# Kernel tuning notes

Hardware: AMD Instinct MI355X
Metric: run time of the kernel (lower is better)

The kernel has to match this reference:

```python
import jax, jax.numpy as jnp
import numpy as np

LN_EPS = 1e-5
BN_EPS = 1e-5


def setup_inputs() -> dict:
    key = jax.random.key(0)
    ks = jax.random.split(key, 16)
    b, n = 16, 256
    sc = 0.1
    inp = {
        "x": jax.random.normal(ks[0], (b, n, 4), jnp.float32),
        # proj: Linear(4, 64)
        "proj_w": jax.random.normal(ks[1], (4, 64), jnp.float32) * sc,
        "proj_b": jnp.zeros((64,), jnp.float32),
        # sigma_net: Linear(128,64) -> LayerNorm(64) -> ReLU -> Linear(64,1) -> Softplus
        "s_w1": jax.random.normal(ks[2], (128, 64), jnp.float32) * sc,
        "s_b1": jnp.zeros((64,), jnp.float32),
        "ln_g": jnp.ones((64,), jnp.float32),
        "ln_b": jnp.zeros((64,), jnp.float32),
        "s_w2": jax.random.normal(ks[3], (64, 1), jnp.float32) * sc,
        "s_b2": jnp.zeros((1,), jnp.float32),
        # gnn weight
        "gnn_w": jax.random.normal(ks[4], (64, 64), jnp.float32) * sc,
        # classifier: Linear(128,64) -> BatchNorm1d(64) -> ELU -> Dropout(eval) -> Linear(64,2)
        "c_w1": jax.random.normal(ks[5], (128, 64), jnp.float32) * sc,
        "c_b1": jnp.zeros((64,), jnp.float32),
        "bn_g": jnp.ones((64,), jnp.float32),
        "bn_b": jnp.zeros((64,), jnp.float32),
        "bn_mean": jnp.zeros((64,), jnp.float32),
        "bn_var": jnp.ones((64,), jnp.float32),
        "c_w2": jax.random.normal(ks[6], (64, 2), jnp.float32) * sc,
        "c_b2": jnp.zeros((2,), jnp.float32),
    }
    return inp


def reference(x, proj_w, proj_b, s_w1, s_b1, ln_g, ln_b, s_w2, s_b2,
              gnn_w, c_w1, c_b1, bn_g, bn_b, bn_mean, bn_var, c_w2, c_b2):
    # h: [b, n, 64]
    h = jax.nn.elu(x @ proj_w + proj_b)

    # sigma_net(cat([xi, xj])) == hi @ s_w1[:64] + hj @ s_w1[64:] + s_b1, broadcast pairwise
    a_i = h @ s_w1[:64]            # [b, n, 64]
    a_j = h @ s_w1[64:]            # [b, n, 64]
    pre = a_i[:, :, None, :] + a_j[:, None, :, :] + s_b1  # [b, n, n, 64]
    mu = jnp.mean(pre, axis=-1, keepdims=True)
    var = jnp.mean((pre - mu) ** 2, axis=-1, keepdims=True)
    ln = (pre - mu) * jax.lax.rsqrt(var + LN_EPS) * ln_g + ln_b
    sig_pre = jax.nn.relu(ln) @ s_w2 + s_b2               # [b, n, n, 1]
    sigmas = jax.nn.softplus(sig_pre[..., 0])             # [b, n, n]

    # squared pairwise distance via gram trick: ||hi - hj||^2
    sq = jnp.sum(h * h, axis=-1)                          # [b, n]
    gram = jnp.einsum("bid,bjd->bij", h, h)               # [b, n, n]
    d2 = jnp.maximum(sq[:, :, None] + sq[:, None, :] - 2.0 * gram, 0.0)
    adj = jnp.exp(-d2 / (2.0 * sigmas ** 2 + 1e-6))       # [b, n, n]

    h_agg = jnp.einsum("bij,bjd->bid", adj, h) @ gnn_w    # [b, n, 64]
    h_res = jax.nn.elu(h_agg + h)

    pooled = jnp.concatenate([h_res.mean(axis=1), h_res.max(axis=1)], axis=1)  # [b, 128]

    z = pooled @ c_w1 + c_b1
    z = (z - bn_mean) * jax.lax.rsqrt(bn_var + BN_EPS) * bn_g + bn_b  # BN eval mode
    z = jax.nn.elu(z)                                      # Dropout is identity in eval
    return z @ c_w2 + c_b2                                 # [b, 2]
```

## Files before the change

kernel.cpp:

```cpp
#include <hip/hip_runtime.h>
#include <math.h>

#define OFF_H      0
#define OFF_AI     262144
#define OFF_AJH    524288
#define OFF_SAI    1048576
#define OFF_QAI    1052672
#define OFF_SAJ    1056768
#define OFF_QAJ    1060864
#define OFF_SQH    1064960
#define OFF_HRES   1069056

__device__ __forceinline__ float fexp(float x)  { return __expf(x); }
__device__ __forceinline__ float flog(float x)  { return __logf(x); }
__device__ __forceinline__ float frcp(float x)  {
    float r = __builtin_amdgcn_rcpf(x);
    return r * (2.f - x * r);
}
__device__ __forceinline__ float frsq(float x)  { return __builtin_amdgcn_rsqf(x); }

__device__ __forceinline__ float elu_f(float x) { return x > 0.f ? x : fexp(x) - 1.f; }
__device__ __forceinline__ float softplus_f(float x) {
    return fmaxf(x, 0.f) + flog(1.f + fexp(-fabsf(x)));
}

__global__ __launch_bounds__(256) void k1_embed(
    const float* __restrict__ x,
    const float* __restrict__ proj_w, const float* __restrict__ proj_b,
    const float* __restrict__ s_w1, const float* __restrict__ s_b1,
    float* __restrict__ h, float* __restrict__ a_i, float2* __restrict__ ajh,
    float* __restrict__ sa_i, float* __restrict__ qa_i,
    float* __restrict__ sa_j, float* __restrict__ qa_j,
    float* __restrict__ sqh)
{
    __shared__ float w_sh[8192];
    int tid = threadIdx.x;
    #pragma unroll
    for (int r = 0; r < 8; ++r)
        *(float4*)&w_sh[(r*256 + tid)*4] = *(const float4*)&s_w1[(r*256 + tid)*4];
    __syncthreads();

    int lane = tid & 63;
    int wave = tid >> 6;
    int row0 = blockIdx.x * 8;

    float pw0 = proj_w[lane], pw1 = proj_w[64+lane], pw2 = proj_w[128+lane],
          pw3 = proj_w[192+lane], pb = proj_b[lane], b1 = s_b1[lane];

    #pragma unroll
    for (int r = 0; r < 2; ++r) {
        int row = row0 + wave*2 + r;
        int b = row >> 8, i = row & 255;
        float4 xv = *(const float4*)&x[row*4];
        float hv = elu_f(xv.x*pw0 + xv.y*pw1 + xv.z*pw2 + xv.w*pw3 + pb);

        float ai = b1, aj = 0.f;
        #pragma unroll 8
        for (int e = 0; e < 64; ++e) {
            float he = __shfl(hv, e);
            ai = fmaf(he, w_sh[e*64 + lane], ai);
            aj = fmaf(he, w_sh[(64+e)*64 + lane], aj);
        }
        h[row*64 + lane]   = hv;
        a_i[row*64 + lane] = ai;
        ajh[b*16384 + lane*256 + i] = make_float2(aj, hv);

        float v1 = ai, v2 = ai*ai, v3 = aj, v4 = aj*aj, v5 = hv*hv;
        #pragma unroll
        for (int off = 32; off > 0; off >>= 1) {
            v1 += __shfl_xor(v1, off);
            v2 += __shfl_xor(v2, off);
            v3 += __shfl_xor(v3, off);
            v4 += __shfl_xor(v4, off);
            v5 += __shfl_xor(v5, off);
        }
        if (lane == 0) {
            sa_i[row] = v1; qa_i[row] = v2;
            sa_j[row] = v3; qa_j[row] = v4;
            sqh[row]  = v5;
        }
    }
}

__global__ __launch_bounds__(256) void k2_pair(
    const float* __restrict__ a_i, const float2* __restrict__ ajh,
    const float* __restrict__ h,
    const float* __restrict__ sa_i, const float* __restrict__ qa_i,
    const float* __restrict__ sa_j, const float* __restrict__ qa_j,
    const float* __restrict__ sqh,
    const float* __restrict__ ln_g, const float* __restrict__ ln_b,
    const float* __restrict__ s_w2, const float* __restrict__ s_b2,
    const float* __restrict__ gnn_w,
    float* __restrict__ h_res)
{
    int bi0 = blockIdx.x * 4;
    int b   = bi0 >> 8;
    int j   = threadIdx.x;
    int gj  = b*256 + j;

    __shared__ float aiT[64][4], hiT[64][4];
    __shared__ float gbw[64][4];
    __shared__ float sai_s[4], qai_s[4], sqi_s[4];
    __shared__ float adj_sh[256][4];
    __shared__ float pool[16*4*64];
    __shared__ float hagg_sh[4][64];

    {
        int i = j >> 6, d = j & 63;
        aiT[d][i] = a_i[(bi0+i)*64 + d];
        hiT[d][i] = h[(bi0+i)*64 + d];
    }
    if (j < 64) {
        gbw[j][0] = ln_g[j]; gbw[j][1] = ln_b[j]; gbw[j][2] = s_w2[j]; gbw[j][3] = 0.f;
    }
    if (j < 4) {
        sai_s[j] = sa_i[bi0+j]; qai_s[j] = qa_i[bi0+j]; sqi_s[j] = sqh[bi0+j];
    }
    float saj = sa_j[gj], qaj = qa_j[gj], sqj = sqh[gj];
    float b2  = s_b2[0];
    __syncthreads();

    const float2* ajhb = ajh + b*16384;

    float ga[4] = {0.f,0.f,0.f,0.f}, gh[4] = {0.f,0.f,0.f,0.f};
    #pragma unroll 8
    for (int d = 0; d < 64; ++d) {
        float2 v = ajhb[d*256 + j];
        float4 A = *(const float4*)&aiT[d][0];
        float4 H = *(const float4*)&hiT[d][0];
        ga[0] = fmaf(A.x, v.x, ga[0]); ga[1] = fmaf(A.y, v.x, ga[1]);
        ga[2] = fmaf(A.z, v.x, ga[2]); ga[3] = fmaf(A.w, v.x, ga[3]);
        gh[0] = fmaf(H.x, v.y, gh[0]); gh[1] = fmaf(H.y, v.y, gh[1]);
        gh[2] = fmaf(H.z, v.y, gh[2]); gh[3] = fmaf(H.w, v.y, gh[3]);
    }

    float rs4[4], nr4[4], d24[4];
    #pragma unroll
    for (int i = 0; i < 4; ++i) {
        float mu  = (sai_s[i] + saj) * (1.f/64.f);
        float pss = qai_s[i] + qaj + 2.f*ga[i];
        float var = pss * (1.f/64.f) - mu*mu;
        rs4[i] = frsq(var + 1e-5f);
        nr4[i] = -mu * rs4[i];
        d24[i] = fmaxf(sqi_s[i] + sqj - 2.f*gh[i], 0.f);
    }

    float acc[4] = {0.f,0.f,0.f,0.f};
    #pragma unroll 8
    for (int d = 0; d < 64; ++d) {
        float ajd = ajhb[d*256 + j].x;
        float4 A = *(const float4*)&aiT[d][0];
        float4 G = *(const float4*)&gbw[d][0];
        float t0 = fmaxf(fmaf(fmaf(A.x + ajd, rs4[0], nr4[0]), G.x, G.y), 0.f);
        acc[0] = fmaf(t0, G.z, acc[0]);
        float t1 = fmaxf(fmaf(fmaf(A.y + ajd, rs4[1], nr4[1]), G.x, G.y), 0.f);
        acc[1] = fmaf(t1, G.z, acc[1]);
        float t2 = fmaxf(fmaf(fmaf(A.z + ajd, rs4[2], nr4[2]), G.x, G.y), 0.f);
        acc[2] = fmaf(t2, G.z, acc[2]);
        float t3 = fmaxf(fmaf(fmaf(A.w + ajd, rs4[3], nr4[3]), G.x, G.y), 0.f);
        acc[3] = fmaf(t3, G.z, acc[3]);
    }

    {
        float4 av;
        #pragma unroll
        for (int i = 0; i < 4; ++i) {
            float sig = softplus_f(acc[i] + b2);
            float inv = frcp(2.f*sig*sig + 1e-6f);
            ((float*)&av)[i] = fexp(-d24[i] * inv);
        }
        *(float4*)&adj_sh[j][0] = av;
    }
    __syncthreads();

    {
        int q = j >> 4, dq = j & 15;
        const float* hb = h + b*256*64;
        float4 p0 = {0.f,0.f,0.f,0.f}, p1 = p0, p2 = p0, p3 = p0;
        #pragma unroll
        for (int k = 0; k < 16; ++k) {
            int jj = q*16 + k;
            float4 hv = *(const float4*)&hb[jj*64 + dq*4];
            float4 a4 = *(const float4*)&adj_sh[jj][0];
            p0.x=fmaf(a4.x,hv.x,p0.x); p0.y=fmaf(a4.x,hv.y,p0.y);
            p0.z=fmaf(a4.x,hv.z,p0.z); p0.w=fmaf(a4.x,hv.w,p0.w);
            p1.x=fmaf(a4.y,hv.x,p1.x); p1.y=fmaf(a4.y,hv.y,p1.y);
            p1.z=fmaf(a4.y,hv.z,p1.z); p1.w=fmaf(a4.y,hv.w,p1.w);
            p2.x=fmaf(a4.z,hv.x,p2.x); p2.y=fmaf(a4.z,hv.y,p2.y);
            p2.z=fmaf(a4.z,hv.z,p2.z); p2.w=fmaf(a4.z,hv.w,p2.w);
            p3.x=fmaf(a4.w,hv.x,p3.x); p3.y=fmaf(a4.w,hv.y,p3.y);
            p3.z=fmaf(a4.w,hv.z,p3.z); p3.w=fmaf(a4.w,hv.w,p3.w);
        }
        *(float4*)&pool[(q*4 + 0)*64 + dq*4] = p0;
        *(float4*)&pool[(q*4 + 1)*64 + dq*4] = p1;
        *(float4*)&pool[(q*4 + 2)*64 + dq*4] = p2;
        *(float4*)&pool[(q*4 + 3)*64 + dq*4] = p3;
    }
    __syncthreads();

    {
        int i = j >> 6, d = j & 63;
        float s = 0.f;
        #pragma unroll
        for (int q2 = 0; q2 < 16; ++q2)
            s += pool[(q2*4 + i)*64 + d];
        hagg_sh[i][d] = s;
    }
    __syncthreads();

    {
        int i = j >> 6, lane = j & 63;
        float accg = 0.f;
        #pragma unroll 8
        for (int e = 0; e < 64; ++e)
            accg = fmaf(hagg_sh[i][e], gnn_w[e*64 + lane], accg);
        h_res[(bi0+i)*64 + lane] = elu_f(accg + hiT[lane][i]);
    }
}

__global__ __launch_bounds__(256) void k4_pool_cls(
    const float* __restrict__ h_res,
    const float* __restrict__ c_w1, const float* __restrict__ c_b1,
    const float* __restrict__ bn_g, const float* __restrict__ bn_b,
    const float* __restrict__ bn_mean, const float* __restrict__ bn_var,
    const float* __restrict__ c_w2, const float* __restrict__ c_b2,
    float* __restrict__ out)
{
    int b = blockIdx.x;
    int tid = threadIdx.x;
    int d = tid & 63, q = tid >> 6;
    const float* hb = h_res + b*256*64;

    float sum = 0.f, mx = -INFINITY;
    #pragma unroll 8
    for (int k = 0; k < 64; ++k) {
        float v = hb[(q*64+k)*64 + d];
        sum += v; mx = fmaxf(mx, v);
    }
    __shared__ float sum_sh[256], max_sh[256];
    __shared__ float pm_sh[64], px_sh[64];
    sum_sh[tid] = sum; max_sh[tid] = mx;
    __syncthreads();
    if (tid < 64) {
        float tsum = sum_sh[tid] + sum_sh[64+tid] + sum_sh[128+tid] + sum_sh[192+tid];
        float tmax = fmaxf(fmaxf(max_sh[tid], max_sh[64+tid]),
                           fmaxf(max_sh[128+tid], max_sh[192+tid]));
        pm_sh[tid] = tsum * (1.f/256.f);
        px_sh[tid] = tmax;
    }
    __syncthreads();
    if (tid < 64) {
        float acc = c_b1[tid];
        #pragma unroll
        for (int e = 0; e < 64; ++e) {
            acc += pm_sh[e] * c_w1[e*64 + tid];
            acc += px_sh[e] * c_w1[(64+e)*64 + tid];
        }
        float z = (acc - bn_mean[tid]) * rsqrtf(bn_var[tid] + 1e-5f) * bn_g[tid] + bn_b[tid];
        z = elu_f(z);
        float c0 = z * c_w2[tid*2 + 0];
        float c1 = z * c_w2[tid*2 + 1];
        for (int off = 32; off > 0; off >>= 1) {
            c0 += __shfl_down(c0, off);
            c1 += __shfl_down(c1, off);
        }
        if (tid == 0) {
            out[b*2 + 0] = c0 + c_b2[0];
            out[b*2 + 1] = c1 + c_b2[1];
        }
    }
}

extern "C" void kernel_launch(void* const* d_in, const int* in_sizes, int n_in,
                              void* d_out, int out_size, void* d_ws, size_t ws_size,
                              hipStream_t stream) {
    const float* x       = (const float*)d_in[0];
    const float* proj_w  = (const float*)d_in[1];
    const float* proj_b  = (const float*)d_in[2];
    const float* s_w1    = (const float*)d_in[3];
    const float* s_b1    = (const float*)d_in[4];
    const float* ln_g    = (const float*)d_in[5];
    const float* ln_b    = (const float*)d_in[6];
    const float* s_w2    = (const float*)d_in[7];
    const float* s_b2    = (const float*)d_in[8];
    const float* gnn_w   = (const float*)d_in[9];
    const float* c_w1    = (const float*)d_in[10];
    const float* c_b1    = (const float*)d_in[11];
    const float* bn_g    = (const float*)d_in[12];
    const float* bn_b    = (const float*)d_in[13];
    const float* bn_mean = (const float*)d_in[14];
    const float* bn_var  = (const float*)d_in[15];
    const float* c_w2    = (const float*)d_in[16];
    const float* c_b2    = (const float*)d_in[17];

    float* w = (float*)d_ws;
    float*  h     = w + OFF_H;
    float*  a_i   = w + OFF_AI;
    float2* ajh   = (float2*)(w + OFF_AJH);
    float*  sa_i  = w + OFF_SAI;
    float*  qa_i  = w + OFF_QAI;
    float*  sa_j  = w + OFF_SAJ;
    float*  qa_j  = w + OFF_QAJ;
    float*  sqh   = w + OFF_SQH;
    float*  h_res = w + OFF_HRES;
    float*  out   = (float*)d_out;

    k1_embed<<<512, 256, 0, stream>>>(x, proj_w, proj_b, s_w1, s_b1,
                                      h, a_i, ajh,
                                      sa_i, qa_i, sa_j, qa_j, sqh);
    k2_pair<<<1024, 256, 0, stream>>>(a_i, ajh, h,
                                      sa_i, qa_i, sa_j, qa_j, sqh,
                                      ln_g, ln_b, s_w2, s_b2, gnn_w, h_res);
    k4_pool_cls<<<16, 256, 0, stream>>>(h_res, c_w1, c_b1, bn_g, bn_b,
                                        bn_mean, bn_var, c_w2, c_b2, out);
}
```

Baseline: 46.26 us.

## Fuse pooling and classifier into pair kernel via last-blocks atomic handoff

Removes the separate pooling/classifier launch. Each pair block increments a global arrival counter, and the last 16 arriving blocks each take one batch's pooling and classifier. Those blocks spin on a flag that the final arrival sets, so every h_res write is visible before they read it. The counter is reset inside the embed kernel. This saves one kernel launch and its inter-kernel gap, at the cost of a serialized tail where 15 blocks busy-wait for the last block.

```diff
diff --git a/kernel.cpp b/kernel.cpp
--- a/kernel.cpp
+++ b/kernel.cpp
@@ -10,6 +10,7 @@
 #define OFF_QAJ    1060864
 #define OFF_SQH    1064960
 #define OFF_HRES   1069056
+#define OFF_SYNC   1331200
 
 __device__ __forceinline__ float fexp(float x)  { return __expf(x); }
 __device__ __forceinline__ float flog(float x)  { return __logf(x); }
@@ -18,7 +19,6 @@
     return r * (2.f - x * r);
 }
 __device__ __forceinline__ float frsq(float x)  { return __builtin_amdgcn_rsqf(x); }
-
 __device__ __forceinline__ float elu_f(float x) { return x > 0.f ? x : fexp(x) - 1.f; }
 __device__ __forceinline__ float softplus_f(float x) {
     return fmaxf(x, 0.f) + flog(1.f + fexp(-fabsf(x)));
@@ -31,8 +31,10 @@
     float* __restrict__ h, float* __restrict__ a_i, float2* __restrict__ ajh,
     float* __restrict__ sa_i, float* __restrict__ qa_i,
     float* __restrict__ sa_j, float* __restrict__ qa_j,
-    float* __restrict__ sqh)
+    float* __restrict__ sqh, unsigned* __restrict__ sync)
 {
+    if (blockIdx.x == 0 && threadIdx.x == 0) { sync[0] = 0u; sync[1] = 0u; }
+
     __shared__ float w_sh[8192];
     int tid = threadIdx.x;
     #pragma unroll
@@ -91,7 +93,12 @@
     const float* __restrict__ ln_g, const float* __restrict__ ln_b,
     const float* __restrict__ s_w2, const float* __restrict__ s_b2,
     const float* __restrict__ gnn_w,
-    float* __restrict__ h_res)
+    const float* __restrict__ c_w1, const float* __restrict__ c_b1,
+    const float* __restrict__ bn_g, const float* __restrict__ bn_b,
+    const float* __restrict__ bn_mean, const float* __restrict__ bn_var,
+    const float* __restrict__ c_w2, const float* __restrict__ c_b2,
+    float* __restrict__ h_res, unsigned* __restrict__ sync,
+    float* __restrict__ out)
 {
     int bi0 = blockIdx.x * 4;
     int b   = bi0 >> 8;
@@ -104,6 +111,7 @@
     __shared__ float adj_sh[256][4];
     __shared__ float pool[16*4*64];
     __shared__ float hagg_sh[4][64];
+    __shared__ unsigned arrival;
 
     {
         int i = j >> 6, d = j & 63;
@@ -216,57 +224,69 @@
             accg = fmaf(hagg_sh[i][e], gnn_w[e*64 + lane], accg);
         h_res[(bi0+i)*64 + lane] = elu_f(accg + hiT[lane][i]);
     }
-}
-
-__global__ __launch_bounds__(256) void k4_pool_cls(
-    const float* __restrict__ h_res,
-    const float* __restrict__ c_w1, const float* __restrict__ c_b1,
-    const float* __restrict__ bn_g, const float* __restrict__ bn_b,
-    const float* __restrict__ bn_mean, const float* __restrict__ bn_var,
-    const float* __restrict__ c_w2, const float* __restrict__ c_b2,
-    float* __restrict__ out)
-{
-    int b = blockIdx.x;
-    int tid = threadIdx.x;
-    int d = tid & 63, q = tid >> 6;
-    const float* hb = h_res + b*256*64;
-
-    float sum = 0.f, mx = -INFINITY;
-    #pragma unroll 8
-    for (int k = 0; k < 64; ++k) {
-        float v = hb[(q*64+k)*64 + d];
-        sum += v; mx = fmaxf(mx, v);
-    }
-    __shared__ float sum_sh[256], max_sh[256];
-    __shared__ float pm_sh[64], px_sh[64];
-    sum_sh[tid] = sum; max_sh[tid] = mx;
-    __syncthreads();
-    if (tid < 64) {
-        float tsum = sum_sh[tid] + sum_sh[64+tid] + sum_sh[128+tid] + sum_sh[192+tid];
-        float tmax = fmaxf(fmaxf(max_sh[tid], max_sh[64+tid]),
-                           fmaxf(max_sh[128+tid], max_sh[192+tid]));
-        pm_sh[tid] = tsum * (1.f/256.f);
-        px_sh[tid] = tmax;
-    }
-    __syncthreads();
-    if (tid < 64) {
-        float acc = c_b1[tid];
-        #pragma unroll
-        for (int e = 0; e < 64; ++e) {
-            acc += pm_sh[e] * c_w1[e*64 + tid];
-            acc += px_sh[e] * c_w1[(64+e)*64 + tid];
-        }
-        float z = (acc - bn_mean[tid]) * rsqrtf(bn_var[tid] + 1e-5f) * bn_g[tid] + bn_b[tid];
-        z = elu_f(z);
-        float c0 = z * c_w2[tid*2 + 0];
-        float c1 = z * c_w2[tid*2 + 1];
-        for (int off = 32; off > 0; off >>= 1) {
-            c0 += __shfl_down(c0, off);
-            c1 += __shfl_down(c1, off);
-        }
-        if (tid == 0) {
-            out[b*2 + 0] = c0 + c_b2[0];
-            out[b*2 + 1] = c1 + c_b2[1];
+
+    __threadfence();
+    if (j == 0) arrival = atomicAdd(&sync[0], 1u);
+    __syncthreads();
+    unsigned a = arrival;
+    if (a < 1008u) return;
+    int bb = (int)(a - 1008u);
+
+    if (j == 0) {
+        if (a == 1023u) {
+            atomicExch(&sync[1], 1u);
+        } else {
+            while (atomicAdd(&sync[1], 0u) == 0u)
+                __builtin_amdgcn_s_sleep(8);
+        }
+    }
+    __syncthreads();
+    __threadfence();
+
+    {
+        float* sum_sh = pool;
+        float* max_sh = pool + 256;
+        float* pm_sh  = pool + 512;
+        float* px_sh  = pool + 576;
+
+        int d = j & 63, q = j >> 6;
+        const float* hb = h_res + bb*256*64;
+
+        float sum = 0.f, mx = -INFINITY;
+        #pragma unroll 8
+        for (int k = 0; k < 64; ++k) {
+            float v = hb[(q*64+k)*64 + d];
+            sum += v; mx = fmaxf(mx, v);
+        }
+        sum_sh[j] = sum; max_sh[j] = mx;
+        __syncthreads();
+        if (j < 64) {
+            float tsum = sum_sh[j] + sum_sh[64+j] + sum_sh[128+j] + sum_sh[192+j];
+            float tmax = fmaxf(fmaxf(max_sh[j], max_sh[64+j]),
+                               fmaxf(max_sh[128+j], max_sh[192+j]));
+            pm_sh[j] = tsum * (1.f/256.f);
+            px_sh[j] = tmax;
+        }
+        __syncthreads();
+        if (j < 64) {
+            float acc2 = c_b1[j];
+            #pragma unroll
+            for (int e = 0; e < 64; ++e) {
+                acc2 += pm_sh[e] * c_w1[e*64 + j];
+                acc2 += px_sh[e] * c_w1[(64+e)*64 + j];
+            }
+            float z = (acc2 - bn_mean[j]) * rsqrtf(bn_var[j] + 1e-5f) * bn_g[j] + bn_b[j];
+            z = elu_f(z);
+            float c0 = z * c_w2[j*2 + 0];
+            float c1 = z * c_w2[j*2 + 1];
+            for (int off = 32; off > 0; off >>= 1) {
+                c0 += __shfl_down(c0, off);
+                c1 += __shfl_down(c1, off);
+            }
+            if (j == 0) {
+                out[bb*2 + 0] = c0 + c_b2[0];
+                out[bb*2 + 1] = c1 + c_b2[1];
+            }
         }
     }
 }
@@ -294,23 +314,24 @@
     const float* c_b2    = (const float*)d_in[17];
 
     float* w = (float*)d_ws;
-    float*  h     = w + OFF_H;
-    float*  a_i   = w + OFF_AI;
-    float2* ajh   = (float2*)(w + OFF_AJH);
-    float*  sa_i  = w + OFF_SAI;
-    float*  qa_i  = w + OFF_QAI;
-    float*  sa_j  = w + OFF_SAJ;
-    float*  qa_j  = w + OFF_QAJ;
-    float*  sqh   = w + OFF_SQH;
-    float*  h_res = w + OFF_HRES;
-    float*  out   = (float*)d_out;
+    float*    h     = w + OFF_H;
+    float*    a_i   = w + OFF_AI;
+    float2*   ajh   = (float2*)(w + OFF_AJH);
+    float*    sa_i  = w + OFF_SAI;
+    float*    qa_i  = w + OFF_QAI;
+    float*    sa_j  = w + OFF_SAJ;
+    float*    qa_j  = w + OFF_QAJ;
+    float*    sqh   = w + OFF_SQH;
+    float*    h_res = w + OFF_HRES;
+    unsigned* sync  = (unsigned*)(w + OFF_SYNC);
+    float*    out   = (float*)d_out;
 
     k1_embed<<<512, 256, 0, stream>>>(x, proj_w, proj_b, s_w1, s_b1,
                                       h, a_i, ajh,
-                                      sa_i, qa_i, sa_j, qa_j, sqh);
+                                      sa_i, qa_i, sa_j, qa_j, sqh, sync);
     k2_pair<<<1024, 256, 0, stream>>>(a_i, ajh, h,
                                       sa_i, qa_i, sa_j, qa_j, sqh,
-                                      ln_g, ln_b, s_w2, s_b2, gnn_w, h_res);
-    k4_pool_cls<<<16, 256, 0, stream>>>(h_res, c_w1, c_b1, bn_g, bn_b,
-                                        bn_mean, bn_var, c_w2, c_b2, out);
-}
+                                      ln_g, ln_b, s_w2, s_b2, gnn_w,
+                                      c_w1, c_b1, bn_g, bn_b, bn_mean, bn_var,
+                                      c_w2, c_b2, h_res, sync, out);
+}
```

Result: slower. 122.7 us (+165.2%).

## Compute pairwise gram matrices with bf16 MFMA in a separate kernel

Applied to the files above, without the earlier changes.

Adds a kgram kernel that computes the a_i·a_j and h·h gram matrices per batch using bf16 MFMA 16x16x32 instructions, writing two full fp32 [b,n,n] matrices to workspace. k1 now also emits bf16 copies of a_i, a_j and h, and k2 reads the precomputed grams instead of running its own 64-step FMA loop. This trades scalar FMA work for matrix-core work plus an extra launch and roughly 8 MB of extra global traffic. Using bf16 for the variance and distance terms lowers precision and risks cancellation error.

```diff
diff --git a/kernel.cpp b/kernel.cpp
--- a/kernel.cpp
+++ b/kernel.cpp
@@ -9,7 +9,13 @@
 #define OFF_SAJ    1056768
 #define OFF_QAJ    1060864
 #define OFF_SQH    1064960
-#define OFF_HRES   1069056
+#define OFF_GA     1069056
+#define OFF_GH     2117632
+#define OFF_HRES   3166208
+#define OFF_BF     3428352
+
+typedef __attribute__((ext_vector_type(8))) short bf16x8;
+typedef __attribute__((ext_vector_type(4))) float f32x4;
 
 __device__ __forceinline__ float fexp(float x)  { return __expf(x); }
 __device__ __forceinline__ float flog(float x)  { return __logf(x); }
@@ -18,10 +24,14 @@
     return r * (2.f - x * r);
 }
 __device__ __forceinline__ float frsq(float x)  { return __builtin_amdgcn_rsqf(x); }
-
 __device__ __forceinline__ float elu_f(float x) { return x > 0.f ? x : fexp(x) - 1.f; }
 __device__ __forceinline__ float softplus_f(float x) {
     return fmaxf(x, 0.f) + flog(1.f + fexp(-fabsf(x)));
+}
+__device__ __forceinline__ short f2bf(float f) {
+    unsigned u = __float_as_uint(f);
+    unsigned r = (u + 0x7FFF + ((u >> 16) & 1)) >> 16;
+    return (short)r;
 }
 
 __global__ __launch_bounds__(256) void k1_embed(
@@ -29,6 +39,7 @@
     const float* __restrict__ proj_w, const float* __restrict__ proj_b,
     const float* __restrict__ s_w1, const float* __restrict__ s_b1,
     float* __restrict__ h, float* __restrict__ a_i, float2* __restrict__ ajh,
+    short* __restrict__ ai_bf, short* __restrict__ aj_bf, short* __restrict__ h_bf,
     float* __restrict__ sa_i, float* __restrict__ qa_i,
     float* __restrict__ sa_j, float* __restrict__ qa_j,
     float* __restrict__ sqh)
@@ -64,6 +75,9 @@
         h[row*64 + lane]   = hv;
         a_i[row*64 + lane] = ai;
         ajh[b*16384 + lane*256 + i] = make_float2(aj, hv);
+        ai_bf[row*64 + lane] = f2bf(ai);
+        aj_bf[row*64 + lane] = f2bf(aj);
+        h_bf [row*64 + lane] = f2bf(hv);
 
         float v1 = ai, v2 = ai*ai, v3 = aj, v4 = aj*aj, v5 = hv*hv;
         #pragma unroll
@@ -82,9 +96,41 @@
     }
 }
 
+__global__ __launch_bounds__(64) void kgram(
+    const short* __restrict__ ai_bf, const short* __restrict__ aj_bf,
+    const short* __restrict__ h_bf,
+    float* __restrict__ ga, float* __restrict__ gh)
+{
+    int bid = blockIdx.x;
+    int g = bid & 1;
+    int s = (bid >> 1) & 15;
+    int b = bid >> 5;
+    const short* XA = (g ? h_bf : ai_bf) + b*256*64;
+    const short* XB = (g ? h_bf : aj_bf) + b*256*64;
+    float* G = (g ? gh : ga) + (b*256 + s*16)*256;
+
+    int l = threadIdx.x, lo = l & 15, hi = l >> 4;
+
+    bf16x8 a0 = *(const bf16x8*)&XA[(s*16 + lo)*64 + hi*8];
+    bf16x8 a1 = *(const bf16x8*)&XA[(s*16 + lo)*64 + 32 + hi*8];
+
+    #pragma unroll 4
+    for (int jt = 0; jt < 16; ++jt) {
+        bf16x8 b0 = *(const bf16x8*)&XB[(jt*16 + lo)*64 + hi*8];
+        bf16x8 b1 = *(const bf16x8*)&XB[(jt*16 + lo)*64 + 32 + hi*8];
+        f32x4 c = {0.f, 0.f, 0.f, 0.f};
+        c = __builtin_amdgcn_mfma_f32_16x16x32_bf16(a0, b0, c, 0, 0, 0);
+        c = __builtin_amdgcn_mfma_f32_16x16x32_bf16(a1, b1, c, 0, 0, 0);
+        #pragma unroll
+        for (int r = 0; r < 4; ++r)
+            G[(hi*4 + r)*256 + jt*16 + lo] = c[r];
+    }
+}
+
 __global__ __launch_bounds__(256) void k2_pair(
     const float* __restrict__ a_i, const float2* __restrict__ ajh,
     const float* __restrict__ h,
+    const float* __restrict__ ga_m, const float* __restrict__ gh_m,
     const float* __restrict__ sa_i, const float* __restrict__ qa_i,
     const float* __restrict__ sa_j, const float* __restrict__ qa_j,
     const float* __restrict__ sqh,
@@ -118,31 +164,25 @@
     }
     float saj = sa_j[gj], qaj = qa_j[gj], sqj = sqh[gj];
     float b2  = s_b2[0];
+    float gav[4], ghv[4];
+    #pragma unroll
+    for (int i = 0; i < 4; ++i) {
+        gav[i] = ga_m[(bi0+i)*256 + j];
+        ghv[i] = gh_m[(bi0+i)*256 + j];
+    }
     __syncthreads();
 
     const float2* ajhb = ajh + b*16384;
-
-    float ga[4] = {0.f,0.f,0.f,0.f}, gh[4] = {0.f,0.f,0.f,0.f};
-    #pragma unroll 8
-    for (int d = 0; d < 64; ++d) {
-        float2 v = ajhb[d*256 + j];
-        float4 A = *(const float4*)&aiT[d][0];
-        float4 H = *(const float4*)&hiT[d][0];
-        ga[0] = fmaf(A.x, v.x, ga[0]); ga[1] = fmaf(A.y, v.x, ga[1]);
-        ga[2] = fmaf(A.z, v.x, ga[2]); ga[3] = fmaf(A.w, v.x, ga[3]);
-        gh[0] = fmaf(H.x, v.y, gh[0]); gh[1] = fmaf(H.y, v.y, gh[1]);
-        gh[2] = fmaf(H.z, v.y, gh[2]); gh[3] = fmaf(H.w, v.y, gh[3]);
-    }
 
     float rs4[4], nr4[4], d24[4];
     #pragma unroll
     for (int i = 0; i < 4; ++i) {
         float mu  = (sai_s[i] + saj) * (1.f/64.f);
-        float pss = qai_s[i] + qaj + 2.f*ga[i];
+        float pss = qai_s[i] + qaj + 2.f*gav[i];
         float var = pss * (1.f/64.f) - mu*mu;
         rs4[i] = frsq(var + 1e-5f);
         nr4[i] = -mu * rs4[i];
-        d24[i] = fmaxf(sqi_s[i] + sqj - 2.f*gh[i], 0.f);
+        d24[i] = fmaxf(sqi_s[i] + sqj - 2.f*ghv[i], 0.f);
     }
 
     float acc[4] = {0.f,0.f,0.f,0.f};
@@ -302,13 +342,19 @@
     float*  sa_j  = w + OFF_SAJ;
     float*  qa_j  = w + OFF_QAJ;
     float*  sqh   = w + OFF_SQH;
+    float*  ga    = w + OFF_GA;
+    float*  gh    = w + OFF_GH;
     float*  h_res = w + OFF_HRES;
+    short*  ai_bf = (short*)(w + OFF_BF);
+    short*  aj_bf = ai_bf + 262144;
+    short*  h_bf  = ai_bf + 524288;
     float*  out   = (float*)d_out;
 
     k1_embed<<<512, 256, 0, stream>>>(x, proj_w, proj_b, s_w1, s_b1,
-                                      h, a_i, ajh,
+                                      h, a_i, ajh, ai_bf, aj_bf, h_bf,
                                       sa_i, qa_i, sa_j, qa_j, sqh);
-    k2_pair<<<1024, 256, 0, stream>>>(a_i, ajh, h,
+    kgram<<<512, 64, 0, stream>>>(ai_bf, aj_bf, h_bf, ga, gh);
+    k2_pair<<<1024, 256, 0, stream>>>(a_i, ajh, h, ga, gh,
                                       sa_i, qa_i, sa_j, qa_j, sqh,
                                       ln_g, ln_b, s_w2, s_b2, gnn_w, h_res);
     k4_pool_cls<<<16, 256, 0, stream>>>(h_res, c_w1, c_b1, bn_g, bn_b,
```

Result: slower. 47.22 us (+2.1%).
